# Kernel tuning notes

Hardware: AMD Instinct MI355X
Metric: run time of the kernel (lower is better)

Reference implementation:

```python
import jax, jax.numpy as jnp
import numpy as np

B, N, C = 4, 2048, 768
H = 12
D = C // H  # head_dim = 64


def setup_inputs() -> dict:
    key = jax.random.key(0)
    k1, k2, k3, k4, k5 = jax.random.split(key, 5)
    s = 0.02
    return {
        "x": jax.random.normal(k1, (B, N, C), dtype=jnp.float32),
        "qkv_w": jax.random.normal(k2, (3 * C, C), dtype=jnp.float32) * s,
        "qkv_b": jax.random.normal(k3, (3 * C,), dtype=jnp.float32) * s,
        "proj_w": jax.random.normal(k4, (C, C), dtype=jnp.float32) * s,
        "proj_b": jax.random.normal(k5, (C,), dtype=jnp.float32) * s,
    }


def reference(x, qkv_w, qkv_b, proj_w, proj_b):
    b, n, c = x.shape
    # qkv projection (torch Linear: x @ W.T + b) -> [B,N,3,H,D] -> [3,B,H,N,D]
    qkv = (x @ qkv_w.T + qkv_b).reshape(b, n, 3, H, D).transpose(2, 0, 3, 1, 4)
    q, k, v = qkv[0], qkv[1], qkv[2]
    scale = D ** (-0.5)
    attn = jnp.einsum("bhqd,bhkd->bhqk", q, k) * scale
    attn = jax.nn.softmax(attn, axis=-1)
    # dropout is identity in eval mode
    out = jnp.einsum("bhqk,bhkd->bhqd", attn, v)  # [B,H,N,D]
    out = out.transpose(0, 2, 1, 3).reshape(b, n, c)
    return out @ proj_w.T + proj_b
```

## Files before the change

kernel.cpp:

```cpp
#include <hip/hip_runtime.h>
#include <hip/hip_bf16.h>
#include <stdint.h>

typedef __bf16 bf16_t;
typedef __bf16 bf16x8 __attribute__((ext_vector_type(8)));
typedef float f32x4 __attribute__((ext_vector_type(4)));
typedef unsigned int u32x4 __attribute__((ext_vector_type(4)));

#define NB 4
#define NH 12
#define ND 64
#define NN 2048
#define NC 768

__device__ __forceinline__ void async_copy16(const bf16_t* g, bf16_t* l) {
    __builtin_amdgcn_global_load_lds((__attribute__((address_space(1))) void*)(void*)g,
                                     (__attribute__((address_space(3))) void*)l, 16, 0, 0);
}

__device__ __forceinline__ unsigned pack_bf2(float a, float b) {
    union { bf16_t e[2]; unsigned u; } t;
    t.e[0] = (bf16_t)a;
    t.e[1] = (bf16_t)b;
    return t.u;
}

__global__ void cast3_kernel(const float* __restrict__ s0, bf16_t* __restrict__ d0, int n0,
                             const float* __restrict__ s1, bf16_t* __restrict__ d1, int n1,
                             const float* __restrict__ s2, bf16_t* __restrict__ d2, int n2) {
    int i = blockIdx.x * blockDim.x + threadIdx.x;
    const float* s;
    bf16_t* d;
    int j;
    if (i < n0)           { s = s0; d = d0; j = i; }
    else if (i < n0 + n1) { s = s1; d = d1; j = i - n0; }
    else if (i < n0 + n1 + n2) { s = s2; d = d2; j = i - n0 - n1; }
    else return;
    float4 v = ((const float4*)s)[j];
    union { bf16_t e[4]; uint2 u; } t;
    t.e[0] = (bf16_t)v.x; t.e[1] = (bf16_t)v.y; t.e[2] = (bf16_t)v.z; t.e[3] = (bf16_t)v.w;
    ((uint2*)d)[j] = t.u;
}

__device__ __forceinline__ int vperm(int s) {
    return (s & 32) | (((s >> 2) & 3) << 3) | (((s >> 4) & 1) << 2) | (s & 3);
}


__launch_bounds__(256)
__global__ void qkv_gemm_kernel(const bf16_t* __restrict__ X, const bf16_t* __restrict__ W,
                                const float* __restrict__ bias,
                                bf16_t* __restrict__ Q, bf16_t* __restrict__ K, bf16_t* __restrict__ V)
{
    __shared__ __align__(16) bf16_t sA[128 * 64];
    __shared__ __align__(16) bf16_t sB[128 * 64];
    const int tid  = threadIdx.x;
    const int lane = tid & 63;
    const int w    = tid >> 6;
    const int wm   = w & 1, wn = w >> 1;
    const int m0   = blockIdx.x * 128;
    const int n0   = blockIdx.y * 128;
    const int lrow = lane & 15;
    const int quad = lane >> 4;
    const int arow = lane >> 3;
    const int gch  = (lane & 7) ^ arow;

    f32x4 zero = {0.f, 0.f, 0.f, 0.f};
    f32x4 acc[4][4];
#pragma unroll
    for (int i = 0; i < 4; ++i)
#pragma unroll
        for (int j = 0; j < 4; ++j) acc[i][j] = zero;

    for (int kt = 0; kt < NC; kt += 64) {
        __syncthreads();
        for (int c = w; c < 16; c += 4) {
            async_copy16(X + (size_t)(m0 + c * 8 + arow) * NC + kt + gch * 8, sA + c * 512);
            async_copy16(W + (size_t)(n0 + c * 8 + arow) * NC + kt + gch * 8, sB + c * 512);
        }
        __syncthreads();
#pragma unroll
        for (int hh = 0; hh < 2; ++hh) {
            bf16x8 af[4], bfr[4];
#pragma unroll
            for (int i = 0; i < 4; ++i) {
                int r = wm * 64 + i * 16 + lrow;
                af[i] = *(const bf16x8*)(sA + r * 64 + (((hh * 4 + quad) ^ (r & 7)) * 8));
            }
#pragma unroll
            for (int j = 0; j < 4; ++j) {
                int r = wn * 64 + j * 16 + lrow;
                bfr[j] = *(const bf16x8*)(sB + r * 64 + (((hh * 4 + quad) ^ (r & 7)) * 8));
            }
#pragma unroll
            for (int i = 0; i < 4; ++i)
#pragma unroll
                for (int j = 0; j < 4; ++j)
                    acc[i][j] = __builtin_amdgcn_mfma_f32_16x16x32_bf16(af[i], bfr[j], acc[i][j], 0, 0, 0);
        }
    }

    const int colbase = n0 + wn * 64;
    const int t3 = colbase / NC;
    const int h  = (colbase % NC) / ND;
    const float qscale = 0.125f * 1.44269504088896340736f;

#pragma unroll
    for (int j = 0; j < 4; ++j) {
        const int d  = j * 16 + lrow;
        const float bv = bias[colbase + d];
#pragma unroll
        for (int i = 0; i < 4; ++i) {
            const int rowg = m0 + wm * 64 + i * 16 + quad * 4;
            const int bb = rowg >> 11;
            const int nn = rowg & 2047;
            if (t3 == 2) {
                union { bf16_t e[4]; uint2 u; } pk;
#pragma unroll
                for (int p = 0; p < 4; ++p) pk.e[p] = (bf16_t)(acc[i][j][p] + bv);
                const int pos = (nn & ~63) | vperm(nn & 63);
                *(uint2*)(V + ((size_t)(bb * NH + h) * ND + d) * NN + pos) = pk.u;
            } else {
                bf16_t* outb = t3 ? K : Q;
#pragma unroll
                for (int p = 0; p < 4; ++p) {
                    float val = acc[i][j][p] + bv;
                    if (t3 == 0) val *= qscale;
                    outb[((size_t)(bb * NH + h) * NN + nn + p) * ND + d] = (bf16_t)val;
                }
            }
        }
    }
}

__launch_bounds__(256, 4)
__global__ void attn_kernel(const bf16_t* __restrict__ Q, const bf16_t* __restrict__ K,
                            const bf16_t* __restrict__ Vt, bf16_t* __restrict__ O)
{
    __shared__ __align__(16) bf16_t sK[2][64 * 64];
    __shared__ __align__(16) bf16_t sV[2][64 * 64];
    bf16_t* sQ = sK[0];
    const int tid  = threadIdx.x;
    const int lane = tid & 63;
    const int w    = tid >> 6;
    const int qt   = blockIdx.x;
    const int h    = blockIdx.y;
    const int b    = blockIdx.z;
    const int lrow = lane & 15;
    const int quad = lane >> 4;
    const int arow = lane >> 3;
    const int gch  = (lane & 7) ^ arow;
    const size_t head_off = (size_t)(b * NH + h) * NN * ND;
    const bf16_t* qh = Q  + head_off;
    const bf16_t* kh = K  + head_off;
    const bf16_t* vh = Vt + head_off;

#pragma unroll
    for (int c = 0; c < 4; ++c)
        async_copy16(qh + (size_t)(qt * 128 + (w * 4 + c) * 8 + arow) * ND + gch * 8,
                     sQ + (w * 4 + c) * 512);
    __syncthreads();

    bf16x8 qb[2][2];
#pragma unroll
    for (int qi = 0; qi < 2; ++qi)
#pragma unroll
        for (int hh = 0; hh < 2; ++hh) {
            int r = w * 32 + qi * 16 + lrow;
            qb[qi][hh] = *(const bf16x8*)(sQ + r * 64 + (((hh * 4 + quad) ^ (r & 7)) * 8));
        }
    __syncthreads();

    bf16x8 ones;
#pragma unroll
    for (int p = 0; p < 8; ++p) ones[p] = (bf16_t)1.0f;

    int off[4][2];
#pragma unroll
    for (int blk = 0; blk < 4; ++blk) {
        int r = blk * 16 + lrow;
        off[blk][0] = r * 64 + ((quad ^ (r & 7)) * 8);
        off[blk][1] = r * 64 + (((4 + quad) ^ (r & 7)) * 8);
    }

    f32x4 zero = {0.f, 0.f, 0.f, 0.f};
    f32x4 o[2][4];
#pragma unroll
    for (int qi = 0; qi < 2; ++qi)
#pragma unroll
        for (int db = 0; db < 4; ++db) o[qi][db] = zero;
    f32x4 lacc[2] = {zero, zero};

    const bf16_t* kp = kh + (size_t)(w * 16 + arow) * ND + gch * 8;
    const bf16_t* vp = vh + (size_t)(w * 16 + arow) * NN + gch * 8;

    async_copy16(kp,          sK[0] + w * 1024);
    async_copy16(kp + 8 * ND, sK[0] + w * 1024 + 512);
    async_copy16(vp,          sV[0] + w * 1024);
    async_copy16(vp + 8 * NN, sV[0] + w * 1024 + 512);
    kp += 64 * ND; vp += 64;
    __syncthreads();

    int cur = 0;
    for (int it = 0; it < NN / 64; ++it) {
        if (it + 1 < NN / 64) {
            bf16_t* dK = sK[cur ^ 1] + w * 1024;
            bf16_t* dV = sV[cur ^ 1] + w * 1024;
            async_copy16(kp,          dK);
            async_copy16(kp + 8 * ND, dK + 512);
            async_copy16(vp,          dV);
            async_copy16(vp + 8 * NN, dV + 512);
            kp += 64 * ND; vp += 64;
        }
        const bf16_t* sKh = sK[cur];
        const bf16_t* sVh = sV[cur];

        f32x4 s[2][4];
#pragma unroll
        for (int blk = 0; blk < 4; ++blk) {
            bf16x8 a0 = *(const bf16x8*)(sKh + off[blk][0]);
            bf16x8 a1 = *(const bf16x8*)(sKh + off[blk][1]);
#pragma unroll
            for (int qi = 0; qi < 2; ++qi) {
                f32x4 z = zero;
                z = __builtin_amdgcn_mfma_f32_16x16x32_bf16(a0, qb[qi][0], z, 0, 0, 0);
                z = __builtin_amdgcn_mfma_f32_16x16x32_bf16(a1, qb[qi][1], z, 0, 0, 0);
                s[qi][blk] = z;
            }
        }

        bf16x8 pe[2][2];
#pragma unroll
        for (int qi = 0; qi < 2; ++qi) {
            u32x4 pu0 = {0, 0, 0, 0}, pu1 = {0, 0, 0, 0};
#pragma unroll
            for (int blk = 0; blk < 4; ++blk) {
                float e0 = __builtin_amdgcn_exp2f(s[qi][blk][0]);
                float e1 = __builtin_amdgcn_exp2f(s[qi][blk][1]);
                float e2 = __builtin_amdgcn_exp2f(s[qi][blk][2]);
                float e3 = __builtin_amdgcn_exp2f(s[qi][blk][3]);
                unsigned lo = pack_bf2(e0, e1), hi = pack_bf2(e2, e3);
                if (blk == 0)      { pu0[0] = lo; pu0[1] = hi; }
                else if (blk == 1) { pu0[2] = lo; pu0[3] = hi; }
                else if (blk == 2) { pu1[0] = lo; pu1[1] = hi; }
                else               { pu1[2] = lo; pu1[3] = hi; }
            }
            pe[qi][0] = __builtin_bit_cast(bf16x8, pu0);
            pe[qi][1] = __builtin_bit_cast(bf16x8, pu1);
            lacc[qi] = __builtin_amdgcn_mfma_f32_16x16x32_bf16(ones, pe[qi][0], lacc[qi], 0, 0, 0);
            lacc[qi] = __builtin_amdgcn_mfma_f32_16x16x32_bf16(ones, pe[qi][1], lacc[qi], 0, 0, 0);
        }

#pragma unroll
        for (int db = 0; db < 4; ++db) {
            bf16x8 v0 = *(const bf16x8*)(sVh + off[db][0]);
            bf16x8 v1 = *(const bf16x8*)(sVh + off[db][1]);
#pragma unroll
            for (int qi = 0; qi < 2; ++qi) {
                o[qi][db] = __builtin_amdgcn_mfma_f32_16x16x32_bf16(v0, pe[qi][0], o[qi][db], 0, 0, 0);
                o[qi][db] = __builtin_amdgcn_mfma_f32_16x16x32_bf16(v1, pe[qi][1], o[qi][db], 0, 0, 0);
            }
        }
        __syncthreads();
        cur ^= 1;
    }

#pragma unroll
    for (int qi = 0; qi < 2; ++qi) {
        const float rl = 1.0f / lacc[qi][0];
        const int n = qt * 128 + w * 32 + qi * 16 + lrow;
        const size_t rowoff = ((size_t)(b * NN + n)) * NC + h * ND;
#pragma unroll
        for (int db = 0; db < 4; ++db) {
            union { bf16_t e[4]; uint2 u; } pk;
#pragma unroll
            for (int p = 0; p < 4; ++p) pk.e[p] = (bf16_t)(o[qi][db][p] * rl);
            *(uint2*)(O + rowoff + db * 16 + quad * 4) = pk.u;
        }
    }
}

__launch_bounds__(256)
__global__ void proj_gemm_kernel(const bf16_t* __restrict__ A, const bf16_t* __restrict__ W,
                                 const float* __restrict__ bias, float* __restrict__ out)
{
    __shared__ __align__(16) bf16_t sA[128 * 64];
    __shared__ __align__(16) bf16_t sB[128 * 64];
    const int tid  = threadIdx.x;
    const int lane = tid & 63;
    const int w    = tid >> 6;
    const int wm   = w & 1, wn = w >> 1;
    const int m0   = blockIdx.x * 128;
    const int n0   = blockIdx.y * 128;
    const int lrow = lane & 15;
    const int quad = lane >> 4;
    const int arow = lane >> 3;
    const int gch  = (lane & 7) ^ arow;

    f32x4 zero = {0.f, 0.f, 0.f, 0.f};
    f32x4 acc[4][4];
#pragma unroll
    for (int i = 0; i < 4; ++i)
#pragma unroll
        for (int j = 0; j < 4; ++j) acc[i][j] = zero;

    for (int kt = 0; kt < NC; kt += 64) {
        __syncthreads();
        for (int c = w; c < 16; c += 4) {
            async_copy16(A + (size_t)(m0 + c * 8 + arow) * NC + kt + gch * 8, sA + c * 512);
            async_copy16(W + (size_t)(n0 + c * 8 + arow) * NC + kt + gch * 8, sB + c * 512);
        }
        __syncthreads();
#pragma unroll
        for (int hh = 0; hh < 2; ++hh) {
            bf16x8 af[4], bfr[4];
#pragma unroll
            for (int i = 0; i < 4; ++i) {
                int r = wm * 64 + i * 16 + lrow;
                af[i] = *(const bf16x8*)(sA + r * 64 + (((hh * 4 + quad) ^ (r & 7)) * 8));
            }
#pragma unroll
            for (int j = 0; j < 4; ++j) {
                int r = wn * 64 + j * 16 + lrow;
                bfr[j] = *(const bf16x8*)(sB + r * 64 + (((hh * 4 + quad) ^ (r & 7)) * 8));
            }
#pragma unroll
            for (int i = 0; i < 4; ++i)
#pragma unroll
                for (int j = 0; j < 4; ++j)
                    acc[i][j] = __builtin_amdgcn_mfma_f32_16x16x32_bf16(af[i], bfr[j], acc[i][j], 0, 0, 0);
        }
    }

#pragma unroll
    for (int j = 0; j < 4; ++j) {
        const int colg = n0 + wn * 64 + j * 16 + lrow;
        const float bv = bias[colg];
#pragma unroll
        for (int i = 0; i < 4; ++i) {
            const int rowg = m0 + wm * 64 + i * 16 + quad * 4;
#pragma unroll
            for (int p = 0; p < 4; ++p)
                out[(size_t)(rowg + p) * NC + colg] = acc[i][j][p] + bv;
        }
    }
}

extern "C" void kernel_launch(void* const* d_in, const int* in_sizes, int n_in,
                              void* d_out, int out_size, void* d_ws, size_t ws_size,
                              hipStream_t stream) {
    const float* x      = (const float*)d_in[0];
    const float* qkv_w  = (const float*)d_in[1];
    const float* qkv_b  = (const float*)d_in[2];
    const float* proj_w = (const float*)d_in[3];
    const float* proj_b = (const float*)d_in[4];
    float* out = (float*)d_out;

    char* ws = (char*)d_ws;
    bf16_t* xb    = (bf16_t*)ws; ws += (size_t)8192 * 768 * 2;
    bf16_t* wqkv  = (bf16_t*)ws; ws += (size_t)2304 * 768 * 2;
    bf16_t* wproj = (bf16_t*)ws; ws += (size_t)768 * 768 * 2;
    bf16_t* qb    = (bf16_t*)ws; ws += (size_t)NB * NH * NN * ND * 2;
    bf16_t* kb    = (bf16_t*)ws; ws += (size_t)NB * NH * NN * ND * 2;
    bf16_t* vb    = (bf16_t*)ws; ws += (size_t)NB * NH * NN * ND * 2;
    bf16_t* ab    = (bf16_t*)ws; ws += (size_t)8192 * 768 * 2;

    const int c0 = 8192 * 768 / 4, c1 = 2304 * 768 / 4, c2 = 768 * 768 / 4;
    cast3_kernel<<<(c0 + c1 + c2 + 255) / 256, 256, 0, stream>>>(x, xb, c0, qkv_w, wqkv, c1, proj_w, wproj, c2);

    qkv_gemm_kernel<<<dim3(8192 / 128, 2304 / 128), 256, 0, stream>>>(xb, wqkv, qkv_b, qb, kb, vb);
    attn_kernel<<<dim3(NN / 128, NH, NB), 256, 0, stream>>>(qb, kb, vb, ab);
    proj_gemm_kernel<<<dim3(8192 / 128, 768 / 128), 256, 0, stream>>>(ab, wproj, proj_b, out);
}
```

Baseline: 210.9 us.

## Use two waves per attention block, each handling 64 query rows

The attention kernel now launches 128 threads (2 waves) per 128-query block instead of 4 waves. Each wave processes 64 query rows, so every K/V fragment read from LDS feeds twice as many MFMAs, and each thread issues more async copies per tile. The exp/pack step is also folded directly after each QK MFMA pair. In exchange, per-thread register use roughly doubles and fewer waves are resident to hide latency, which could hurt occupancy.

```diff
diff --git a/kernel.cpp b/kernel.cpp
--- a/kernel.cpp
+++ b/kernel.cpp
@@ -133,7 +133,7 @@
     }
 }
 
-__launch_bounds__(256, 4)
+__launch_bounds__(128, 2)
 __global__ void attn_kernel(const bf16_t* __restrict__ Q, const bf16_t* __restrict__ K,
                             const bf16_t* __restrict__ Vt, bf16_t* __restrict__ O)
 {
@@ -156,17 +156,17 @@
     const bf16_t* vh = Vt + head_off;
 
 #pragma unroll
-    for (int c = 0; c < 4; ++c)
-        async_copy16(qh + (size_t)(qt * 128 + (w * 4 + c) * 8 + arow) * ND + gch * 8,
-                     sQ + (w * 4 + c) * 512);
+    for (int c = 0; c < 8; ++c)
+        async_copy16(qh + (size_t)(qt * 128 + (w * 8 + c) * 8 + arow) * ND + gch * 8,
+                     sQ + (w * 8 + c) * 512);
     __syncthreads();
 
-    bf16x8 qb[2][2];
-#pragma unroll
-    for (int qi = 0; qi < 2; ++qi)
+    bf16x8 qb[4][2];
+#pragma unroll
+    for (int qi = 0; qi < 4; ++qi)
 #pragma unroll
         for (int hh = 0; hh < 2; ++hh) {
-            int r = w * 32 + qi * 16 + lrow;
+            int r = w * 64 + qi * 16 + lrow;
             qb[qi][hh] = *(const bf16x8*)(sQ + r * 64 + (((hh * 4 + quad) ^ (r & 7)) * 8));
         }
     __syncthreads();
@@ -184,69 +184,61 @@
     }
 
     f32x4 zero = {0.f, 0.f, 0.f, 0.f};
-    f32x4 o[2][4];
-#pragma unroll
-    for (int qi = 0; qi < 2; ++qi)
+    f32x4 o[4][4];
+#pragma unroll
+    for (int qi = 0; qi < 4; ++qi)
 #pragma unroll
         for (int db = 0; db < 4; ++db) o[qi][db] = zero;
-    f32x4 lacc[2] = {zero, zero};
-
-    const bf16_t* kp = kh + (size_t)(w * 16 + arow) * ND + gch * 8;
-    const bf16_t* vp = vh + (size_t)(w * 16 + arow) * NN + gch * 8;
-
-    async_copy16(kp,          sK[0] + w * 1024);
-    async_copy16(kp + 8 * ND, sK[0] + w * 1024 + 512);
-    async_copy16(vp,          sV[0] + w * 1024);
-    async_copy16(vp + 8 * NN, sV[0] + w * 1024 + 512);
+    f32x4 lacc[4] = {zero, zero, zero, zero};
+
+    const bf16_t* kp = kh + (size_t)(w * 32 + arow) * ND + gch * 8;
+    const bf16_t* vp = vh + (size_t)(w * 32 + arow) * NN + gch * 8;
+
+#pragma unroll
+    for (int c = 0; c < 4; ++c) {
+        async_copy16(kp + (size_t)c * 8 * ND, sK[0] + w * 2048 + c * 512);
+        async_copy16(vp + (size_t)c * 8 * NN, sV[0] + w * 2048 + c * 512);
+    }
     kp += 64 * ND; vp += 64;
     __syncthreads();
 
     int cur = 0;
     for (int it = 0; it < NN / 64; ++it) {
         if (it + 1 < NN / 64) {
-            bf16_t* dK = sK[cur ^ 1] + w * 1024;
-            bf16_t* dV = sV[cur ^ 1] + w * 1024;
-            async_copy16(kp,          dK);
-            async_copy16(kp + 8 * ND, dK + 512);
-            async_copy16(vp,          dV);
-            async_copy16(vp + 8 * NN, dV + 512);
+            bf16_t* dK = sK[cur ^ 1] + w * 2048;
+            bf16_t* dV = sV[cur ^ 1] + w * 2048;
+#pragma unroll
+            for (int c = 0; c < 4; ++c) {
+                async_copy16(kp + (size_t)c * 8 * ND, dK + c * 512);
+                async_copy16(vp + (size_t)c * 8 * NN, dV + c * 512);
+            }
             kp += 64 * ND; vp += 64;
         }
         const bf16_t* sKh = sK[cur];
         const bf16_t* sVh = sV[cur];
 
-        f32x4 s[2][4];
+        u32x4 pu[4][2];
 #pragma unroll
         for (int blk = 0; blk < 4; ++blk) {
             bf16x8 a0 = *(const bf16x8*)(sKh + off[blk][0]);
             bf16x8 a1 = *(const bf16x8*)(sKh + off[blk][1]);
 #pragma unroll
-            for (int qi = 0; qi < 2; ++qi) {
+            for (int qi = 0; qi < 4; ++qi) {
                 f32x4 z = zero;
                 z = __builtin_amdgcn_mfma_f32_16x16x32_bf16(a0, qb[qi][0], z, 0, 0, 0);
                 z = __builtin_amdgcn_mfma_f32_16x16x32_bf16(a1, qb[qi][1], z, 0, 0, 0);
-                s[qi][blk] = z;
-            }
-        }
-
-        bf16x8 pe[2][2];
-#pragma unroll
-        for (int qi = 0; qi < 2; ++qi) {
-            u32x4 pu0 = {0, 0, 0, 0}, pu1 = {0, 0, 0, 0};
-#pragma unroll
-            for (int blk = 0; blk < 4; ++blk) {
-                float e0 = __builtin_amdgcn_exp2f(s[qi][blk][0]);
-                float e1 = __builtin_amdgcn_exp2f(s[qi][blk][1]);
-                float e2 = __builtin_amdgcn_exp2f(s[qi][blk][2]);
-                float e3 = __builtin_amdgcn_exp2f(s[qi][blk][3]);
-                unsigned lo = pack_bf2(e0, e1), hi = pack_bf2(e2, e3);
-                if (blk == 0)      { pu0[0] = lo; pu0[1] = hi; }
-                else if (blk == 1) { pu0[2] = lo; pu0[3] = hi; }
-                else if (blk == 2) { pu1[0] = lo; pu1[1] = hi; }
-                else               { pu1[2] = lo; pu1[3] = hi; }
-            }
-            pe[qi][0] = __builtin_bit_cast(bf16x8, pu0);
-            pe[qi][1] = __builtin_bit_cast(bf16x8, pu1);
+                unsigned lo = pack_bf2(__builtin_amdgcn_exp2f(z[0]), __builtin_amdgcn_exp2f(z[1]));
+                unsigned hi = pack_bf2(__builtin_amdgcn_exp2f(z[2]), __builtin_amdgcn_exp2f(z[3]));
+                pu[qi][blk >> 1][(blk & 1) * 2]     = lo;
+                pu[qi][blk >> 1][(blk & 1) * 2 + 1] = hi;
+            }
+        }
+
+        bf16x8 pe[4][2];
+#pragma unroll
+        for (int qi = 0; qi < 4; ++qi) {
+            pe[qi][0] = __builtin_bit_cast(bf16x8, pu[qi][0]);
+            pe[qi][1] = __builtin_bit_cast(bf16x8, pu[qi][1]);
             lacc[qi] = __builtin_amdgcn_mfma_f32_16x16x32_bf16(ones, pe[qi][0], lacc[qi], 0, 0, 0);
             lacc[qi] = __builtin_amdgcn_mfma_f32_16x16x32_bf16(ones, pe[qi][1], lacc[qi], 0, 0, 0);
         }
@@ -256,7 +248,7 @@
             bf16x8 v0 = *(const bf16x8*)(sVh + off[db][0]);
             bf16x8 v1 = *(const bf16x8*)(sVh + off[db][1]);
 #pragma unroll
-            for (int qi = 0; qi < 2; ++qi) {
+            for (int qi = 0; qi < 4; ++qi) {
                 o[qi][db] = __builtin_amdgcn_mfma_f32_16x16x32_bf16(v0, pe[qi][0], o[qi][db], 0, 0, 0);
                 o[qi][db] = __builtin_amdgcn_mfma_f32_16x16x32_bf16(v1, pe[qi][1], o[qi][db], 0, 0, 0);
             }
@@ -266,9 +258,9 @@
     }
 
 #pragma unroll
-    for (int qi = 0; qi < 2; ++qi) {
+    for (int qi = 0; qi < 4; ++qi) {
         const float rl = 1.0f / lacc[qi][0];
-        const int n = qt * 128 + w * 32 + qi * 16 + lrow;
+        const int n = qt * 128 + w * 64 + qi * 16 + lrow;
         const size_t rowoff = ((size_t)(b * NN + n)) * NC + h * ND;
 #pragma unroll
         for (int db = 0; db < 4; ++db) {
@@ -369,6 +361,6 @@
     cast3_kernel<<<(c0 + c1 + c2 + 255) / 256, 256, 0, stream>>>(x, xb, c0, qkv_w, wqkv, c1, proj_w, wproj, c2);
 
     qkv_gemm_kernel<<<dim3(8192 / 128, 2304 / 128), 256, 0, stream>>>(xb, wqkv, qkv_b, qb, kb, vb);
-    attn_kernel<<<dim3(NN / 128, NH, NB), 256, 0, stream>>>(qb, kb, vb, ab);
+    attn_kernel<<<dim3(NN / 128, NH, NB), 128, 0, stream>>>(qb, kb, vb, ab);
     proj_gemm_kernel<<<dim3(8192 / 128, 768 / 128), 256, 0, stream>>>(ab, wproj, proj_b, out);
 }
```

Result: slower. 230.1 us (+9.1%).

## Load K/V fragments directly from global memory, drop LDS staging and barriers

Applied to the files above, without the earlier changes.

The attention kernel no longer stages Q, K and V tiles through double-buffered shared memory with async copies and __syncthreads. Each wave now loads its MFMA operand fragments straight from global memory into registers, relying on L1/L2 caching because all four waves of a block read the same K/V tiles. It also raises wave priority around the MFMA sections and lowers the occupancy hint from 4 to 3 blocks to leave room for the extra fragment registers. The cost is redundant global traffic across waves and loads that are no longer prefetched, so memory latency is exposed on every iteration.

```diff
diff --git a/kernel.cpp b/kernel.cpp
--- a/kernel.cpp
+++ b/kernel.cpp
@@ -133,13 +133,10 @@
     }
 }
 
-__launch_bounds__(256, 4)
+__launch_bounds__(256, 3)
 __global__ void attn_kernel(const bf16_t* __restrict__ Q, const bf16_t* __restrict__ K,
                             const bf16_t* __restrict__ Vt, bf16_t* __restrict__ O)
 {
-    __shared__ __align__(16) bf16_t sK[2][64 * 64];
-    __shared__ __align__(16) bf16_t sV[2][64 * 64];
-    bf16_t* sQ = sK[0];
     const int tid  = threadIdx.x;
     const int lane = tid & 63;
     const int w    = tid >> 6;
@@ -148,40 +145,22 @@
     const int b    = blockIdx.z;
     const int lrow = lane & 15;
     const int quad = lane >> 4;
-    const int arow = lane >> 3;
-    const int gch  = (lane & 7) ^ arow;
     const size_t head_off = (size_t)(b * NH + h) * NN * ND;
     const bf16_t* qh = Q  + head_off;
     const bf16_t* kh = K  + head_off;
     const bf16_t* vh = Vt + head_off;
 
-#pragma unroll
-    for (int c = 0; c < 4; ++c)
-        async_copy16(qh + (size_t)(qt * 128 + (w * 4 + c) * 8 + arow) * ND + gch * 8,
-                     sQ + (w * 4 + c) * 512);
-    __syncthreads();
-
     bf16x8 qb[2][2];
 #pragma unroll
     for (int qi = 0; qi < 2; ++qi)
 #pragma unroll
-        for (int hh = 0; hh < 2; ++hh) {
-            int r = w * 32 + qi * 16 + lrow;
-            qb[qi][hh] = *(const bf16x8*)(sQ + r * 64 + (((hh * 4 + quad) ^ (r & 7)) * 8));
-        }
-    __syncthreads();
+        for (int hh = 0; hh < 2; ++hh)
+            qb[qi][hh] = *(const bf16x8*)(qh + (size_t)(qt * 128 + w * 32 + qi * 16 + lrow) * ND
+                                             + hh * 32 + quad * 8);
 
     bf16x8 ones;
 #pragma unroll
     for (int p = 0; p < 8; ++p) ones[p] = (bf16_t)1.0f;
-
-    int off[4][2];
-#pragma unroll
-    for (int blk = 0; blk < 4; ++blk) {
-        int r = blk * 16 + lrow;
-        off[blk][0] = r * 64 + ((quad ^ (r & 7)) * 8);
-        off[blk][1] = r * 64 + (((4 + quad) ^ (r & 7)) * 8);
-    }
 
     f32x4 zero = {0.f, 0.f, 0.f, 0.f};
     f32x4 o[2][4];
@@ -191,43 +170,38 @@
         for (int db = 0; db < 4; ++db) o[qi][db] = zero;
     f32x4 lacc[2] = {zero, zero};
 
-    const bf16_t* kp = kh + (size_t)(w * 16 + arow) * ND + gch * 8;
-    const bf16_t* vp = vh + (size_t)(w * 16 + arow) * NN + gch * 8;
-
-    async_copy16(kp,          sK[0] + w * 1024);
-    async_copy16(kp + 8 * ND, sK[0] + w * 1024 + 512);
-    async_copy16(vp,          sV[0] + w * 1024);
-    async_copy16(vp + 8 * NN, sV[0] + w * 1024 + 512);
-    kp += 64 * ND; vp += 64;
-    __syncthreads();
-
-    int cur = 0;
+    const bf16_t* kpl = kh + (size_t)lrow * ND + quad * 8;
+    const bf16_t* vpl = vh + (size_t)lrow * NN + quad * 8;
+
     for (int it = 0; it < NN / 64; ++it) {
-        if (it + 1 < NN / 64) {
-            bf16_t* dK = sK[cur ^ 1] + w * 1024;
-            bf16_t* dV = sV[cur ^ 1] + w * 1024;
-            async_copy16(kp,          dK);
-            async_copy16(kp + 8 * ND, dK + 512);
-            async_copy16(vp,          dV);
-            async_copy16(vp + 8 * NN, dV + 512);
-            kp += 64 * ND; vp += 64;
-        }
-        const bf16_t* sKh = sK[cur];
-        const bf16_t* sVh = sV[cur];
+        bf16x8 kf[4][2];
+#pragma unroll
+        for (int blk = 0; blk < 4; ++blk)
+#pragma unroll
+            for (int hh = 0; hh < 2; ++hh)
+                kf[blk][hh] = *(const bf16x8*)(kpl + blk * 16 * ND + hh * 32);
+        bf16x8 vf[4][2];
+#pragma unroll
+        for (int db = 0; db < 4; ++db)
+#pragma unroll
+            for (int hh = 0; hh < 2; ++hh)
+                vf[db][hh] = *(const bf16x8*)(vpl + db * 16 * NN + hh * 32);
+        kpl += (size_t)64 * ND;
+        vpl += 64;
 
         f32x4 s[2][4];
+        __builtin_amdgcn_s_setprio(1);
 #pragma unroll
         for (int blk = 0; blk < 4; ++blk) {
-            bf16x8 a0 = *(const bf16x8*)(sKh + off[blk][0]);
-            bf16x8 a1 = *(const bf16x8*)(sKh + off[blk][1]);
 #pragma unroll
             for (int qi = 0; qi < 2; ++qi) {
                 f32x4 z = zero;
-                z = __builtin_amdgcn_mfma_f32_16x16x32_bf16(a0, qb[qi][0], z, 0, 0, 0);
-                z = __builtin_amdgcn_mfma_f32_16x16x32_bf16(a1, qb[qi][1], z, 0, 0, 0);
+                z = __builtin_amdgcn_mfma_f32_16x16x32_bf16(kf[blk][0], qb[qi][0], z, 0, 0, 0);
+                z = __builtin_amdgcn_mfma_f32_16x16x32_bf16(kf[blk][1], qb[qi][1], z, 0, 0, 0);
                 s[qi][blk] = z;
             }
         }
+        __builtin_amdgcn_s_setprio(0);
 
         bf16x8 pe[2][2];
 #pragma unroll
@@ -247,22 +221,23 @@
             }
             pe[qi][0] = __builtin_bit_cast(bf16x8, pu0);
             pe[qi][1] = __builtin_bit_cast(bf16x8, pu1);
+        }
+
+        __builtin_amdgcn_s_setprio(1);
+#pragma unroll
+        for (int qi = 0; qi < 2; ++qi) {
             lacc[qi] = __builtin_amdgcn_mfma_f32_16x16x32_bf16(ones, pe[qi][0], lacc[qi], 0, 0, 0);
             lacc[qi] = __builtin_amdgcn_mfma_f32_16x16x32_bf16(ones, pe[qi][1], lacc[qi], 0, 0, 0);
         }
-
 #pragma unroll
         for (int db = 0; db < 4; ++db) {
-            bf16x8 v0 = *(const bf16x8*)(sVh + off[db][0]);
-            bf16x8 v1 = *(const bf16x8*)(sVh + off[db][1]);
 #pragma unroll
             for (int qi = 0; qi < 2; ++qi) {
-                o[qi][db] = __builtin_amdgcn_mfma_f32_16x16x32_bf16(v0, pe[qi][0], o[qi][db], 0, 0, 0);
-                o[qi][db] = __builtin_amdgcn_mfma_f32_16x16x32_bf16(v1, pe[qi][1], o[qi][db], 0, 0, 0);
-            }
-        }
-        __syncthreads();
-        cur ^= 1;
+                o[qi][db] = __builtin_amdgcn_mfma_f32_16x16x32_bf16(vf[db][0], pe[qi][0], o[qi][db], 0, 0, 0);
+                o[qi][db] = __builtin_amdgcn_mfma_f32_16x16x32_bf16(vf[db][1], pe[qi][1], o[qi][db], 0, 0, 0);
+            }
+        }
+        __builtin_amdgcn_s_setprio(0);
     }
 
 #pragma unroll
```

After: 321.6 us. 52.5% more time.

## Triple-buffer K/V in attention with fine-grained vmcnt waits and setprio

Applied to the files above, without the earlier changes.

Changes the attention kernel's K/V LDS staging from double to triple buffering. Loads are issued two tiles ahead, and each iteration waits with an explicit s_waitcnt vmcnt(4) plus a raw s_barrier instead of a full __syncthreads drain. MFMA phases are wrapped in s_setprio to favour matrix work over exp. It uses 50% more LDS and lowers launch bounds from 4 to 3 blocks per CU, which may reduce occupancy.

```diff
diff --git a/kernel.cpp b/kernel.cpp
--- a/kernel.cpp
+++ b/kernel.cpp
@@ -133,12 +133,86 @@
     }
 }
 
-__launch_bounds__(256, 4)
+#define WAIT_BAR(N)                                              \
+    asm volatile("s_waitcnt vmcnt(" #N ")" ::: "memory");        \
+    __builtin_amdgcn_sched_barrier(0);                           \
+    __builtin_amdgcn_s_barrier();                                \
+    __builtin_amdgcn_sched_barrier(0);
+
+#define STAGE(BUF)                                               \
+    {                                                            \
+        bf16_t* dK = sK[BUF] + w * 1024;                         \
+        bf16_t* dV = sV[BUF] + w * 1024;                         \
+        async_copy16(kp,          dK);                           \
+        async_copy16(kp + 8 * ND, dK + 512);                     \
+        async_copy16(vp,          dV);                           \
+        async_copy16(vp + 8 * NN, dV + 512);                     \
+        kp += (size_t)64 * ND; vp += 64;                         \
+    }
+
+#define ATTN_COMPUTE(CUR)                                                                            \
+    {                                                                                                \
+        const bf16_t* sKh = sK[CUR];                                                                 \
+        const bf16_t* sVh = sV[CUR];                                                                 \
+        f32x4 s[2][4];                                                                               \
+        __builtin_amdgcn_s_setprio(1);                                                               \
+        _Pragma("unroll")                                                                            \
+        for (int blk = 0; blk < 4; ++blk) {                                                          \
+            bf16x8 a0 = *(const bf16x8*)(sKh + off[blk][0]);                                         \
+            bf16x8 a1 = *(const bf16x8*)(sKh + off[blk][1]);                                         \
+            _Pragma("unroll")                                                                        \
+            for (int qi = 0; qi < 2; ++qi) {                                                         \
+                f32x4 z = zero;                                                                      \
+                z = __builtin_amdgcn_mfma_f32_16x16x32_bf16(a0, qb[qi][0], z, 0, 0, 0);              \
+                z = __builtin_amdgcn_mfma_f32_16x16x32_bf16(a1, qb[qi][1], z, 0, 0, 0);              \
+                s[qi][blk] = z;                                                                      \
+            }                                                                                        \
+        }                                                                                            \
+        __builtin_amdgcn_s_setprio(0);                                                               \
+        bf16x8 pe[2][2];                                                                             \
+        _Pragma("unroll")                                                                            \
+        for (int qi = 0; qi < 2; ++qi) {                                                             \
+            u32x4 pu0 = {0, 0, 0, 0}, pu1 = {0, 0, 0, 0};                                            \
+            _Pragma("unroll")                                                                        \
+            for (int blk = 0; blk < 4; ++blk) {                                                      \
+                float e0 = __builtin_amdgcn_exp2f(s[qi][blk][0]);                                    \
+                float e1 = __builtin_amdgcn_exp2f(s[qi][blk][1]);                                    \
+                float e2 = __builtin_amdgcn_exp2f(s[qi][blk][2]);                                    \
+                float e3 = __builtin_amdgcn_exp2f(s[qi][blk][3]);                                    \
+                unsigned lo = pack_bf2(e0, e1), hi = pack_bf2(e2, e3);                               \
+                if (blk == 0)      { pu0[0] = lo; pu0[1] = hi; }                                     \
+                else if (blk == 1) { pu0[2] = lo; pu0[3] = hi; }                                     \
+                else if (blk == 2) { pu1[0] = lo; pu1[1] = hi; }                                     \
+                else               { pu1[2] = lo; pu1[3] = hi; }                                     \
+            }                                                                                        \
+            pe[qi][0] = __builtin_bit_cast(bf16x8, pu0);                                             \
+            pe[qi][1] = __builtin_bit_cast(bf16x8, pu1);                                             \
+        }                                                                                            \
+        __builtin_amdgcn_s_setprio(1);                                                               \
+        _Pragma("unroll")                                                                            \
+        for (int qi = 0; qi < 2; ++qi) {                                                             \
+            lacc[qi] = __builtin_amdgcn_mfma_f32_16x16x32_bf16(ones, pe[qi][0], lacc[qi], 0, 0, 0);  \
+            lacc[qi] = __builtin_amdgcn_mfma_f32_16x16x32_bf16(ones, pe[qi][1], lacc[qi], 0, 0, 0);  \
+        }                                                                                            \
+        _Pragma("unroll")                                                                            \
+        for (int db = 0; db < 4; ++db) {                                                             \
+            bf16x8 v0 = *(const bf16x8*)(sVh + off[db][0]);                                          \
+            bf16x8 v1 = *(const bf16x8*)(sVh + off[db][1]);                                          \
+            _Pragma("unroll")                                                                        \
+            for (int qi = 0; qi < 2; ++qi) {                                                         \
+                o[qi][db] = __builtin_amdgcn_mfma_f32_16x16x32_bf16(v0, pe[qi][0], o[qi][db], 0, 0, 0); \
+                o[qi][db] = __builtin_amdgcn_mfma_f32_16x16x32_bf16(v1, pe[qi][1], o[qi][db], 0, 0, 0); \
+            }                                                                                        \
+        }                                                                                            \
+        __builtin_amdgcn_s_setprio(0);                                                               \
+    }
+
+__launch_bounds__(256, 3)
 __global__ void attn_kernel(const bf16_t* __restrict__ Q, const bf16_t* __restrict__ K,
                             const bf16_t* __restrict__ Vt, bf16_t* __restrict__ O)
 {
-    __shared__ __align__(16) bf16_t sK[2][64 * 64];
-    __shared__ __align__(16) bf16_t sV[2][64 * 64];
+    __shared__ __align__(16) bf16_t sK[3][64 * 64];
+    __shared__ __align__(16) bf16_t sV[3][64 * 64];
     bf16_t* sQ = sK[0];
     const int tid  = threadIdx.x;
     const int lane = tid & 63;
@@ -194,76 +268,22 @@
     const bf16_t* kp = kh + (size_t)(w * 16 + arow) * ND + gch * 8;
     const bf16_t* vp = vh + (size_t)(w * 16 + arow) * NN + gch * 8;
 
-    async_copy16(kp,          sK[0] + w * 1024);
-    async_copy16(kp + 8 * ND, sK[0] + w * 1024 + 512);
-    async_copy16(vp,          sV[0] + w * 1024);
-    async_copy16(vp + 8 * NN, sV[0] + w * 1024 + 512);
-    kp += 64 * ND; vp += 64;
-    __syncthreads();
+    STAGE(0);
+    STAGE(1);
+    WAIT_BAR(4);
 
     int cur = 0;
-    for (int it = 0; it < NN / 64; ++it) {
-        if (it + 1 < NN / 64) {
-            bf16_t* dK = sK[cur ^ 1] + w * 1024;
-            bf16_t* dV = sV[cur ^ 1] + w * 1024;
-            async_copy16(kp,          dK);
-            async_copy16(kp + 8 * ND, dK + 512);
-            async_copy16(vp,          dV);
-            async_copy16(vp + 8 * NN, dV + 512);
-            kp += 64 * ND; vp += 64;
-        }
-        const bf16_t* sKh = sK[cur];
-        const bf16_t* sVh = sV[cur];
-
-        f32x4 s[2][4];
-#pragma unroll
-        for (int blk = 0; blk < 4; ++blk) {
-            bf16x8 a0 = *(const bf16x8*)(sKh + off[blk][0]);
-            bf16x8 a1 = *(const bf16x8*)(sKh + off[blk][1]);
-#pragma unroll
-            for (int qi = 0; qi < 2; ++qi) {
-                f32x4 z = zero;
-                z = __builtin_amdgcn_mfma_f32_16x16x32_bf16(a0, qb[qi][0], z, 0, 0, 0);
-                z = __builtin_amdgcn_mfma_f32_16x16x32_bf16(a1, qb[qi][1], z, 0, 0, 0);
-                s[qi][blk] = z;
-            }
-        }
-
-        bf16x8 pe[2][2];
-#pragma unroll
-        for (int qi = 0; qi < 2; ++qi) {
-            u32x4 pu0 = {0, 0, 0, 0}, pu1 = {0, 0, 0, 0};
-#pragma unroll
-            for (int blk = 0; blk < 4; ++blk) {
-                float e0 = __builtin_amdgcn_exp2f(s[qi][blk][0]);
-                float e1 = __builtin_amdgcn_exp2f(s[qi][blk][1]);
-                float e2 = __builtin_amdgcn_exp2f(s[qi][blk][2]);
-                float e3 = __builtin_amdgcn_exp2f(s[qi][blk][3]);
-                unsigned lo = pack_bf2(e0, e1), hi = pack_bf2(e2, e3);
-                if (blk == 0)      { pu0[0] = lo; pu0[1] = hi; }
-                else if (blk == 1) { pu0[2] = lo; pu0[3] = hi; }
-                else if (blk == 2) { pu1[0] = lo; pu1[1] = hi; }
-                else               { pu1[2] = lo; pu1[3] = hi; }
-            }
-            pe[qi][0] = __builtin_bit_cast(bf16x8, pu0);
-            pe[qi][1] = __builtin_bit_cast(bf16x8, pu1);
-            lacc[qi] = __builtin_amdgcn_mfma_f32_16x16x32_bf16(ones, pe[qi][0], lacc[qi], 0, 0, 0);
-            lacc[qi] = __builtin_amdgcn_mfma_f32_16x16x32_bf16(ones, pe[qi][1], lacc[qi], 0, 0, 0);
-        }
-
-#pragma unroll
-        for (int db = 0; db < 4; ++db) {
-            bf16x8 v0 = *(const bf16x8*)(sVh + off[db][0]);
-            bf16x8 v1 = *(const bf16x8*)(sVh + off[db][1]);
-#pragma unroll
-            for (int qi = 0; qi < 2; ++qi) {
-                o[qi][db] = __builtin_amdgcn_mfma_f32_16x16x32_bf16(v0, pe[qi][0], o[qi][db], 0, 0, 0);
-                o[qi][db] = __builtin_amdgcn_mfma_f32_16x16x32_bf16(v1, pe[qi][1], o[qi][db], 0, 0, 0);
-            }
-        }
-        __syncthreads();
-        cur ^= 1;
-    }
+    for (int it = 0; it < NN / 64 - 2; ++it) {
+        int nxt = cur + 2; if (nxt >= 3) nxt -= 3;
+        STAGE(nxt);
+        ATTN_COMPUTE(cur);
+        WAIT_BAR(4);
+        cur = (cur + 1 == 3) ? 0 : cur + 1;
+    }
+    ATTN_COMPUTE(cur);
+    WAIT_BAR(0);
+    cur = (cur + 1 == 3) ? 0 : cur + 1;
+    ATTN_COMPUTE(cur);
 
 #pragma unroll
     for (int qi = 0; qi < 2; ++qi) {
```

Measured after the change: 212.0 us. No clear change (+0.5%).
